# Kernel optimization log

Hardware: AMD Instinct MI355X
Metric: run time of the kernel (lower is better)

## Reference

```python
import jax, jax.numpy as jnp
import numpy as np

DIM = 96
EXPANSION = 2
INNER = DIM * EXPANSION        # 192
QKV_BLOCK = 4                  # per-head dim DH
NH = INNER // QKV_BLOCK        # 48 heads
CONV_K = 4
B, H, W = 2, 24, 24
EPS = 1e-5


def setup_inputs() -> dict:
    key = jax.random.key(0)
    ks = jax.random.split(key, 10)
    nrm = lambda k, shape, s=0.02: jax.random.normal(k, shape, dtype=jnp.float32) * s
    return {
        "x": jax.random.normal(ks[0], (B, DIM, H, W), dtype=jnp.float32),
        "ln_g": jnp.ones((DIM,), jnp.float32),
        "ln_b": jnp.zeros((DIM,), jnp.float32),
        "w_up": nrm(ks[1], (2 * INNER, DIM)),
        "b_up": jnp.zeros((2 * INNER,), jnp.float32),
        "w_q": nrm(ks[2], (NH, QKV_BLOCK, QKV_BLOCK), 0.2),
        "b_q": jnp.zeros((INNER,), jnp.float32),
        "w_k": nrm(ks[3], (NH, QKV_BLOCK, QKV_BLOCK), 0.2),
        "b_k": jnp.zeros((INNER,), jnp.float32),
        "w_v": nrm(ks[4], (NH, QKV_BLOCK, QKV_BLOCK), 0.2),
        "b_v": jnp.zeros((INNER,), jnp.float32),
        "w_conv": nrm(ks[5], (INNER, 1, CONV_K), 0.1),  # depthwise (O,I/g,K)
        "b_conv": jnp.zeros((INNER,), jnp.float32),
        "w_ig": nrm(ks[6], (NH, 3 * INNER)),
        "b_ig": jnp.zeros((NH,), jnp.float32),
        "w_fg": jnp.zeros((NH, 3 * INNER), jnp.float32),
        "b_fg": jnp.linspace(3.0, 6.0, NH, dtype=jnp.float32),  # xLSTM fgate bias init
        "on_g": jnp.ones((INNER,), jnp.float32),
        "on_b": jnp.zeros((INNER,), jnp.float32),
        "skip": jnp.ones((INNER,), jnp.float32),
        "w_down": nrm(ks[7], (DIM, INNER)),
        "b_down": jnp.zeros((DIM,), jnp.float32),
    }


def _layernorm(x, g, b):
    m = x.mean(-1, keepdims=True)
    v = x.var(-1, keepdims=True)
    return (x - m) / jnp.sqrt(v + EPS) * g + b


def _causal_conv(x, w, b):
    # x: (B,S,D); depthwise causal conv1d, left-pad K-1
    y = jax.lax.conv_general_dilated(
        x.transpose(0, 2, 1), w, (1,), [(CONV_K - 1, 0)],
        feature_group_count=INNER, dimension_numbers=("NCH", "OIH", "NCH"))
    return y.transpose(0, 2, 1) + b


def _headwise(x, w, b):
    # LinearHeadwiseExpand: block-diagonal per-head linear
    Bq, S, _ = x.shape
    xh = x.reshape(Bq, S, NH, QKV_BLOCK)
    return jnp.einsum("bsnd,nod->bsno", xh, w).reshape(Bq, S, INNER) + b


def _mlstm(q, k, v, ig, fg):
    # parallel_stabilized_simple; q,k,v: (B,NH,S,DH); ig,fg: (B,NH,S)
    S, DH = q.shape[2], q.shape[3]
    log_f = jax.nn.log_sigmoid(fg)                                           # (B,NH,S)
    lf_cum = jnp.concatenate(
        [jnp.zeros_like(log_f[..., :1]), jnp.cumsum(log_f, axis=-1)], axis=-1)  # (B,NH,S+1)
    log_fmat = lf_cum[..., :, None] - lf_cum[..., None, :]                   # (B,NH,S+1,S+1)
    ltr = jnp.tril(jnp.ones((S, S), dtype=bool))
    log_fg_mat = jnp.where(ltr, log_fmat[..., 1:, 1:], -jnp.inf)             # (B,NH,S,S)
    log_D = log_fg_mat + ig[..., None, :]
    max_log_D = jnp.max(log_D, axis=-1, keepdims=True)                       # rowwise stabilizer
    Dm = jnp.exp(log_D - max_log_D)
    qk = jnp.einsum("bhsd,bhtd->bhst", q, k) * (DH ** -0.5)
    Cm = qk * Dm
    normalizer = jnp.maximum(jnp.abs(Cm.sum(-1, keepdims=True)), jnp.exp(-max_log_D))
    return jnp.einsum("bhst,bhtd->bhsd", Cm / (normalizer + 1e-6), v)


def _mh_norm(h, g, b):
    # MultiHeadLayerNorm: per-head normalization over DH, then full affine
    m = h.mean(-1, keepdims=True)
    v = h.var(-1, keepdims=True)
    hn = (h - m) / jnp.sqrt(v + EPS)
    return hn * g.reshape(1, NH, 1, QKV_BLOCK) + b.reshape(1, NH, 1, QKV_BLOCK)


def reference(x, ln_g, ln_b, w_up, b_up, w_q, b_q, w_k, b_k, w_v, b_v,
              w_conv, b_conv, w_ig, b_ig, w_fg, b_fg, on_g, on_b, skip,
              w_down, b_down):
    Bb, C, Hh, Ww = x.shape
    S = Hh * Ww
    xs = x.reshape(Bb, C, S).transpose(0, 2, 1)                 # (B,S,C)
    h = _layernorm(xs, ln_g, ln_b)                              # ViLBlock pre-LN
    xi = h @ w_up.T + b_up                                      # (B,S,2*INNER)
    x_mlstm, z = jnp.split(xi, 2, axis=-1)
    x_conv = jax.nn.silu(_causal_conv(x_mlstm, w_conv, b_conv))
    q = _headwise(x_conv, w_q, b_q)
    k = _headwise(x_conv, w_k, b_k)
    v = _headwise(x_mlstm, w_v, b_v)
    qkv = jnp.concatenate([q, k, v], axis=-1)                   # (B,S,3*INNER)
    ig = jnp.einsum("bsf,hf->bhs", qkv, w_ig) + b_ig[None, :, None]
    fg = jnp.einsum("bsf,hf->bhs", qkv, w_fg) + b_fg[None, :, None]
    to_heads = lambda t: t.reshape(Bb, S, NH, QKV_BLOCK).transpose(0, 2, 1, 3)
    h_tilde = _mlstm(to_heads(q), to_heads(k), to_heads(v), ig, fg)   # (B,NH,S,DH)
    h_norm = _mh_norm(h_tilde, on_g, on_b).transpose(0, 2, 1, 3).reshape(Bb, S, INNER)
    h_skip = h_norm + skip * x_conv
    h_state = h_skip * jax.nn.silu(z)
    out = h_state @ w_down.T + b_down
    y = xs + out                                                # ViLBlock residual
    return y.transpose(0, 2, 1).reshape(Bb, C, Hh, Ww)
```

## Files before the change

kernel.cpp:

```cpp
#include <hip/hip_runtime.h>
#include <math.h>

#define SEQ   576
#define CDIM  96
#define INNER 192
#define NHEAD 48
#define DH    4
#define NB    2
#define EPSV  1e-5f
#define RT    64

__device__ __forceinline__ float silu_f(float x) { return x / (1.f + __expf(-x)); }
__device__ __forceinline__ float logsig_f(float x) {
    return (x >= 0.f) ? -log1pf(__expf(-x)) : (x - log1pf(__expf(x)));
}

__global__ void __launch_bounds__(512) k_ln_up(const float* __restrict__ x,
    const float* __restrict__ ln_g, const float* __restrict__ ln_b,
    const float* __restrict__ w_up, const float* __restrict__ b_up,
    float* __restrict__ xm, float* __restrict__ z) {
    const int t = threadIdx.x;
    const int p0 = blockIdx.x * 8;
    const int b = p0 / SEQ;
    const int f0 = blockIdx.y * 192;
    __shared__ __align__(16) float hbuf[8][CDIM];

    {
        const int p = t >> 6, l = t & 63;
        const int s = (p0 + p) % SEQ;
        const float v0 = x[(size_t)(b * CDIM + l) * SEQ + s];
        const float v1 = (l < 32) ? x[(size_t)(b * CDIM + 64 + l) * SEQ + s] : 0.f;
        float sum = v0 + v1, sq = v0 * v0 + v1 * v1;
        #pragma unroll
        for (int off = 1; off < 64; off <<= 1) {
            sum += __shfl_xor(sum, off);
            sq  += __shfl_xor(sq, off);
        }
        const float mean = sum * (1.f / CDIM);
        const float var = sq * (1.f / CDIM) - mean * mean;
        const float rstd = rsqrtf(var + EPSV);
        hbuf[p][l] = (v0 - mean) * rstd * ln_g[l] + ln_b[l];
        if (l < 32) hbuf[p][64 + l] = (v1 - mean) * rstd * ln_g[64 + l] + ln_b[64 + l];
    }
    __syncthreads();

    const int lane = t & 7, oi = t >> 3;
    const int p2 = oi & 7, fg = oi >> 3;
    const int pos = p0 + p2;
    const float4* hr = (const float4*)(&hbuf[p2][0]) + lane * 3;
    const float4 h0 = hr[0], h1 = hr[1], h2 = hr[2];
    #pragma unroll 4
    for (int j = 0; j < 24; ++j) {
        const int f = f0 + fg + 8 * j;
        const float4* wr = (const float4*)(w_up + (size_t)f * CDIM) + lane * 3;
        float4 w0 = wr[0], w1 = wr[1], w2 = wr[2];
        float acc = h0.x * w0.x + h0.y * w0.y + h0.z * w0.z + h0.w * w0.w
                  + h1.x * w1.x + h1.y * w1.y + h1.z * w1.z + h1.w * w1.w
                  + h2.x * w2.x + h2.y * w2.y + h2.z * w2.z + h2.w * w2.w;
        #pragma unroll
        for (int off = 1; off < 8; off <<= 1) acc += __shfl_xor(acc, off);
        if (lane == 0) {
            acc += b_up[f];
            if (f < INNER) xm[(size_t)pos * INNER + f] = acc;
            else           z [(size_t)pos * INNER + (f - INNER)] = acc;
        }
    }
}

__global__ void __launch_bounds__(512) k_conv_qkv_gates(const float* __restrict__ xm,
    const float* __restrict__ w_conv, const float* __restrict__ b_conv,
    const float* __restrict__ w_q, const float* __restrict__ b_q,
    const float* __restrict__ w_k, const float* __restrict__ b_k,
    const float* __restrict__ w_v, const float* __restrict__ b_v,
    const float* __restrict__ w_ig, const float* __restrict__ b_ig,
    const float* __restrict__ w_fg, const float* __restrict__ b_fg,
    float* __restrict__ xc, float* __restrict__ qw, float* __restrict__ kw,
    float* __restrict__ vw, float* __restrict__ igw, float* __restrict__ fgw) {
    const int t = threadIdx.x;
    const int p0 = blockIdx.x * 4;
    const int b = p0 / SEQ, s0 = p0 % SEQ;
    __shared__ float xmb[7][INNER];
    __shared__ float xcb[4][INNER];
    __shared__ __align__(16) float qkvb[4][3 * INNER];

    for (int i = t; i < 7 * INNER; i += 512) {
        const int r = i / INNER, c = i % INNER;
        const int ss = s0 - 3 + r;
        xmb[r][c] = (ss >= 0) ? xm[(size_t)(b * SEQ + ss) * INNER + c] : 0.f;
    }
    __syncthreads();

    for (int i = t; i < 4 * INNER; i += 512) {
        const int p = i / INNER, c = i % INNER;
        float acc = b_conv[c];
        #pragma unroll
        for (int j = 0; j < 4; ++j) acc += xmb[p + j][c] * w_conv[c * 4 + j];
        const float v = silu_f(acc);
        xcb[p][c] = v;
        xc[(size_t)(b * SEQ + s0 + p) * INNER + c] = v;
    }
    __syncthreads();

    for (int i = t; i < 4 * INNER; i += 512) {
        const int p = i / INNER, c = i % INNER;
        const int n = c >> 2, o = c & 3;
        const float* wq = w_q + n * 16 + o * 4;
        const float* wk = w_k + n * 16 + o * 4;
        const float* wv = w_v + n * 16 + o * 4;
        float q = b_q[c], k = b_k[c], v = b_v[c];
        #pragma unroll
        for (int dd = 0; dd < 4; ++dd) {
            q += xcb[p][n * 4 + dd] * wq[dd];
            k += xcb[p][n * 4 + dd] * wk[dd];
            v += xmb[p + 3][n * 4 + dd] * wv[dd];
        }
        qkvb[p][c] = q; qkvb[p][INNER + c] = k; qkvb[p][2 * INNER + c] = v;
        const size_t base = ((size_t)(b * NHEAD + n) * SEQ + s0 + p) * DH + o;
        qw[base] = q; kw[base] = k; vw[base] = v;
    }
    __syncthreads();

    {
        const int w = t >> 6;
        const int l16 = t & 15, gg = (t >> 4) & 3;
        #pragma unroll
        for (int it = 0; it < 3; ++it) {
            const int g = w * 12 + it * 4 + gg;
            const bool isfg = (g >= NHEAD);
            const int hh = isfg ? (g - NHEAD) : g;
            const float4* wr = (const float4*)((isfg ? w_fg : w_ig) + (size_t)hh * (3 * INNER)) + l16 * 9;
            float4 wf[9];
            #pragma unroll
            for (int j = 0; j < 9; ++j) wf[j] = wr[j];
            #pragma unroll
            for (int p = 0; p < 4; ++p) {
                const float4* xr = (const float4*)(&qkvb[p][0]) + l16 * 9;
                float acc = 0.f;
                #pragma unroll
                for (int j = 0; j < 9; ++j) {
                    const float4 a = xr[j];
                    acc += a.x * wf[j].x + a.y * wf[j].y + a.z * wf[j].z + a.w * wf[j].w;
                }
                #pragma unroll
                for (int off = 1; off < 16; off <<= 1) acc += __shfl_xor(acc, off);
                if (l16 == 0) {
                    acc += isfg ? b_fg[hh] : b_ig[hh];
                    (isfg ? fgw : igw)[((size_t)b * NHEAD + hh) * SEQ + s0 + p] = acc;
                }
            }
        }
    }
}

__global__ void __launch_bounds__(256) k_mlstm(const float* __restrict__ qw,
    const float* __restrict__ kw, const float* __restrict__ vw,
    const float* __restrict__ igw, const float* __restrict__ fgw,
    float* __restrict__ ht) {
    const int bh = blockIdx.x;
    const int r0 = blockIdx.y * RT;
    const int nt = r0 + RT;
    const int t = threadIdx.x;
    __shared__ float4 k4[SEQ], v4[SEQ];
    __shared__ float m_l[SEQ], M_l[SEQ], lfc_l[SEQ];

    const float4* kb = (const float4*)(kw + (size_t)bh * SEQ * DH);
    const float4* vb = (const float4*)(vw + (size_t)bh * SEQ * DH);
    for (int i = t; i < nt; i += 256) { k4[i] = kb[i]; v4[i] = vb[i]; }

    if (t < 64) {
        const int base = t * 9;
        float pre[9], mv[9], mx[9];
        float run = 0.f;
        #pragma unroll
        for (int j = 0; j < 9; ++j) {
            run += logsig_f(fgw[(size_t)bh * SEQ + base + j]);
            pre[j] = run;
        }
        float incl = run;
        #pragma unroll
        for (int off = 1; off < 64; off <<= 1) {
            float o = __shfl_up(incl, off);
            if (t >= off) incl += o;
        }
        const float excl = incl - run;
        float runm = -INFINITY;
        #pragma unroll
        for (int j = 0; j < 9; ++j) {
            float lfc = excl + pre[j];
            lfc_l[base + j] = lfc;
            float mt = igw[(size_t)bh * SEQ + base + j] - lfc;
            mv[j] = mt;
            runm = fmaxf(runm, mt);
            mx[j] = runm;
        }
        float sc = runm;
        #pragma unroll
        for (int off = 1; off < 64; off <<= 1) {
            float o = __shfl_up(sc, off);
            if (t >= off) sc = fmaxf(sc, o);
        }
        float exclm = __shfl_up(sc, 1);
        if (t == 0) exclm = -INFINITY;
        #pragma unroll
        for (int j = 0; j < 9; ++j) {
            m_l[base + j] = mv[j];
            M_l[base + j] = fmaxf(exclm, mx[j]);
        }
    }
    __syncthreads();

    const int sub = t & 3;
    const int s0 = r0 + (t >> 2);
    const float4 q = ((const float4*)(qw + (size_t)bh * SEQ * DH))[s0];
    const float Ms = M_l[s0], lfcs = lfc_l[s0];

    float a0 = 0.f, a1 = 0.f, a2 = 0.f, a3 = 0.f, csum = 0.f;
    for (int tt = sub; tt <= s0; tt += 4) {
        float e = __expf(m_l[tt] - Ms);
        float4 kk = k4[tt], vv = v4[tt];
        float qk = q.x * kk.x + q.y * kk.y + q.z * kk.z + q.w * kk.w;
        float c = qk * 0.5f * e;
        csum += c;
        a0 += c * vv.x; a1 += c * vv.y; a2 += c * vv.z; a3 += c * vv.w;
    }
    #pragma unroll
    for (int off = 1; off < 4; off <<= 1) {
        csum += __shfl_xor(csum, off);
        a0 += __shfl_xor(a0, off); a1 += __shfl_xor(a1, off);
        a2 += __shfl_xor(a2, off); a3 += __shfl_xor(a3, off);
    }
    const float floorv = __expf(-(lfcs + Ms));
    const float inv = 1.f / (fmaxf(fabsf(csum), floorv) + 1e-6f);
    const float val = (sub == 0) ? a0 : (sub == 1) ? a1 : (sub == 2) ? a2 : a3;
    ht[((size_t)bh * SEQ + s0) * 4 + sub] = val * inv;
}

__global__ void __launch_bounds__(512) k_epi(const float* __restrict__ ht,
    const float* __restrict__ on_g, const float* __restrict__ on_b,
    const float* __restrict__ skip, const float* __restrict__ xc,
    const float* __restrict__ zz, const float* __restrict__ w_down,
    const float* __restrict__ b_down, const float* __restrict__ x,
    float* __restrict__ out) {
    const int t = threadIdx.x;
    const int p0 = blockIdx.x * 4;
    const int b = p0 / SEQ;
    __shared__ __align__(16) float hs[4][INNER];

    for (int i = t; i < 4 * INNER; i += 512) {
        const int p = i / INNER, c = i % INNER;
        const int pos = p0 + p, s = pos % SEQ;
        const int n = c >> 2, o = c & 3;
        const float4 hv = ((const float4*)ht)[(size_t)(b * NHEAD + n) * SEQ + s];
        const float mean = (hv.x + hv.y + hv.z + hv.w) * 0.25f;
        const float d0 = hv.x - mean, d1 = hv.y - mean, d2 = hv.z - mean, d3 = hv.w - mean;
        const float var = (d0 * d0 + d1 * d1 + d2 * d2 + d3 * d3) * 0.25f;
        const float rstd = rsqrtf(var + EPSV);
        const float he = (o == 0) ? hv.x : (o == 1) ? hv.y : (o == 2) ? hv.z : hv.w;
        const float hn = (he - mean) * rstd * on_g[c] + on_b[c];
        const float hk = hn + skip[c] * xc[(size_t)pos * INNER + c];
        hs[p][c] = hk * silu_f(zz[(size_t)pos * INNER + c]);
    }
    __syncthreads();

    const int lane = t & 7, oi = t >> 3;
    const int p2 = oi & 3, cg = oi >> 2;
    const int pos = p0 + p2, s = pos % SEQ;
    const float4* hr = (const float4*)(&hs[p2][0]) + lane * 6;
    float4 h4[6];
    #pragma unroll
    for (int j = 0; j < 6; ++j) h4[j] = hr[j];
    #pragma unroll
    for (int j = 0; j < 6; ++j) {
        const int c = cg + 16 * j;
        const float4* wr = (const float4*)(w_down + (size_t)c * INNER) + lane * 6;
        float acc = 0.f;
        #pragma unroll
        for (int u = 0; u < 6; ++u) {
            const float4 w = wr[u];
            acc += h4[u].x * w.x + h4[u].y * w.y + h4[u].z * w.z + h4[u].w * w.w;
        }
        #pragma unroll
        for (int off = 1; off < 8; off <<= 1) acc += __shfl_xor(acc, off);
        if (lane == 0) {
            const size_t idx = ((size_t)b * CDIM + c) * SEQ + s;
            out[idx] = x[idx] + acc + b_down[c];
        }
    }
}

extern "C" void kernel_launch(void* const* d_in, const int* in_sizes, int n_in,
                              void* d_out, int out_size, void* d_ws, size_t ws_size,
                              hipStream_t stream) {
    const float* x      = (const float*)d_in[0];
    const float* ln_g   = (const float*)d_in[1];
    const float* ln_b   = (const float*)d_in[2];
    const float* w_up   = (const float*)d_in[3];
    const float* b_up   = (const float*)d_in[4];
    const float* w_q    = (const float*)d_in[5];
    const float* b_q    = (const float*)d_in[6];
    const float* w_k    = (const float*)d_in[7];
    const float* b_k    = (const float*)d_in[8];
    const float* w_v    = (const float*)d_in[9];
    const float* b_v    = (const float*)d_in[10];
    const float* w_conv = (const float*)d_in[11];
    const float* b_conv = (const float*)d_in[12];
    const float* w_ig   = (const float*)d_in[13];
    const float* b_ig   = (const float*)d_in[14];
    const float* w_fg   = (const float*)d_in[15];
    const float* b_fg   = (const float*)d_in[16];
    const float* on_g   = (const float*)d_in[17];
    const float* on_b   = (const float*)d_in[18];
    const float* skip   = (const float*)d_in[19];
    const float* w_down = (const float*)d_in[20];
    const float* b_down = (const float*)d_in[21];

    float* ws = (float*)d_ws;
    const size_t NSI = (size_t)NB * SEQ * INNER;
    const size_t NHS = (size_t)NB * NHEAD * SEQ;
    float* xm  = ws;
    float* z   = xm + NSI;
    float* xc  = z + NSI;
    float* qw  = xc + NSI;
    float* kw  = qw + NSI;
    float* vw  = kw + NSI;
    float* igw = vw + NSI;
    float* fgw = igw + NHS;
    float* ht  = fgw + NHS;

    float* out = (float*)d_out;

    hipLaunchKernelGGL(k_ln_up, dim3(NB * SEQ / 8, 2), dim3(512), 0, stream,
                       x, ln_g, ln_b, w_up, b_up, xm, z);
    hipLaunchKernelGGL(k_conv_qkv_gates, dim3(NB * SEQ / 4), dim3(512), 0, stream,
                       xm, w_conv, b_conv, w_q, b_q, w_k, b_k, w_v, b_v,
                       w_ig, b_ig, w_fg, b_fg, xc, qw, kw, vw, igw, fgw);
    hipLaunchKernelGGL(k_mlstm, dim3(NB * NHEAD, SEQ / RT), dim3(256), 0, stream,
                       qw, kw, vw, igw, fgw, ht);
    hipLaunchKernelGGL(k_epi, dim3(NB * SEQ / 4), dim3(512), 0, stream,
                       ht, on_g, on_b, skip, xc, z, w_down, b_down, x, out);
}
```

Baseline: 60.31 us.

## Fuse four stages into one persistent cooperative kernel with grid syncs

Merges the LN+up-projection, conv/qkv/gates, mLSTM and epilogue kernels into a single cooperative kernel of 288 blocks separated by grid.sync(), removing three launch gaps. The mLSTM phase is rebalanced so each block handles three row tiles of one head, chosen so every block gets a roughly equal share of the causal triangle. Each stage now runs on fewer, smaller blocks (256 threads), and grid-wide barriers add their own cost, so per-stage parallelism drops.

```diff
diff --git a/kernel.cpp b/kernel.cpp
--- a/kernel.cpp
+++ b/kernel.cpp
@@ -1,4 +1,5 @@
 #include <hip/hip_runtime.h>
+#include <hip/hip_cooperative_groups.h>
 #include <math.h>
 
 #define SEQ   576
@@ -8,282 +9,280 @@
 #define DH    4
 #define NB    2
 #define EPSV  1e-5f
-#define RT    64
+
+namespace cg = cooperative_groups;
 
 __device__ __forceinline__ float silu_f(float x) { return x / (1.f + __expf(-x)); }
 __device__ __forceinline__ float logsig_f(float x) {
     return (x >= 0.f) ? -log1pf(__expf(-x)) : (x - log1pf(__expf(x)));
 }
 
-__global__ void __launch_bounds__(512) k_ln_up(const float* __restrict__ x,
-    const float* __restrict__ ln_g, const float* __restrict__ ln_b,
-    const float* __restrict__ w_up, const float* __restrict__ b_up,
-    float* __restrict__ xm, float* __restrict__ z) {
+struct Params {
+    const float *x, *ln_g, *ln_b, *w_up, *b_up;
+    const float *w_q, *b_q, *w_k, *b_k, *w_v, *b_v;
+    const float *w_conv, *b_conv;
+    const float *w_ig, *b_ig, *w_fg, *b_fg;
+    const float *on_g, *on_b, *skip, *w_down, *b_down;
+    float *xm, *z, *xc, *qw, *kw, *vw, *igw, *fgw, *ht, *out;
+};
+
+__global__ void __launch_bounds__(256, 2) k_vil(Params P) {
     const int t = threadIdx.x;
-    const int p0 = blockIdx.x * 8;
-    const int b = p0 / SEQ;
-    const int f0 = blockIdx.y * 192;
-    __shared__ __align__(16) float hbuf[8][CDIM];
+    const int blk = blockIdx.x;
+    __shared__ __align__(16) float smem[6336];
+    cg::grid_group grid = cg::this_grid();
 
     {
-        const int p = t >> 6, l = t & 63;
-        const int s = (p0 + p) % SEQ;
-        const float v0 = x[(size_t)(b * CDIM + l) * SEQ + s];
-        const float v1 = (l < 32) ? x[(size_t)(b * CDIM + 64 + l) * SEQ + s] : 0.f;
-        float sum = v0 + v1, sq = v0 * v0 + v1 * v1;
+        float* hbuf = smem;
+        const int p0 = blk * 4;
+        const int b = p0 / SEQ;
+        {
+            const int p = t >> 6, l = t & 63;
+            const int s = (p0 + p) % SEQ;
+            const float v0 = P.x[(size_t)(b * CDIM + l) * SEQ + s];
+            const float v1 = (l < 32) ? P.x[(size_t)(b * CDIM + 64 + l) * SEQ + s] : 0.f;
+            float sum = v0 + v1, sq = v0 * v0 + v1 * v1;
+            #pragma unroll
+            for (int off = 1; off < 64; off <<= 1) {
+                sum += __shfl_xor(sum, off);
+                sq  += __shfl_xor(sq, off);
+            }
+            const float mean = sum * (1.f / CDIM);
+            const float rstd = rsqrtf(sq * (1.f / CDIM) - mean * mean + EPSV);
+            hbuf[p * CDIM + l] = (v0 - mean) * rstd * P.ln_g[l] + P.ln_b[l];
+            if (l < 32) hbuf[p * CDIM + 64 + l] = (v1 - mean) * rstd * P.ln_g[64 + l] + P.ln_b[64 + l];
+        }
+        __syncthreads();
+        const int lane = t & 7, oi = t >> 3;
+        const int p2 = oi & 3, fg = oi >> 2;
+        const int pos = p0 + p2;
+        const float4* hr = (const float4*)(hbuf + p2 * CDIM) + lane * 3;
+        const float4 h0 = hr[0], h1 = hr[1], h2 = hr[2];
+        #pragma unroll 4
+        for (int j = 0; j < 48; ++j) {
+            const int f = fg + 8 * j;
+            const float4* wr = (const float4*)(P.w_up + (size_t)f * CDIM) + lane * 3;
+            const float4 w0 = wr[0], w1 = wr[1], w2 = wr[2];
+            float acc = h0.x*w0.x + h0.y*w0.y + h0.z*w0.z + h0.w*w0.w
+                      + h1.x*w1.x + h1.y*w1.y + h1.z*w1.z + h1.w*w1.w
+                      + h2.x*w2.x + h2.y*w2.y + h2.z*w2.z + h2.w*w2.w;
+            #pragma unroll
+            for (int off = 1; off < 8; off <<= 1) acc += __shfl_xor(acc, off);
+            if (lane == 0) {
+                acc += P.b_up[f];
+                if (f < INNER) P.xm[(size_t)pos * INNER + f] = acc;
+                else           P.z [(size_t)pos * INNER + (f - INNER)] = acc;
+            }
+        }
+    }
+    grid.sync();
+
+    {
+        float* xmb  = smem;
+        float* xcb  = smem + 7 * INNER;
+        float* qkvb = smem + 11 * INNER;
+        const int p0 = blk * 4;
+        const int b = p0 / SEQ, s0 = p0 % SEQ;
+
+        for (int i = t; i < 7 * INNER; i += 256) {
+            const int r = i / INNER, c = i % INNER;
+            const int ss = s0 - 3 + r;
+            xmb[i] = (ss >= 0) ? P.xm[(size_t)(b * SEQ + ss) * INNER + c] : 0.f;
+        }
+        __syncthreads();
+        for (int i = t; i < 4 * INNER; i += 256) {
+            const int p = i / INNER, c = i % INNER;
+            float acc = P.b_conv[c];
+            #pragma unroll
+            for (int j = 0; j < 4; ++j) acc += xmb[(p + j) * INNER + c] * P.w_conv[c * 4 + j];
+            const float v = silu_f(acc);
+            xcb[i] = v;
+            P.xc[(size_t)(p0 + p) * INNER + c] = v;
+        }
+        __syncthreads();
+        for (int i = t; i < 4 * INNER; i += 256) {
+            const int p = i / INNER, c = i % INNER;
+            const int n = c >> 2, o = c & 3;
+            const float* wq = P.w_q + n * 16 + o * 4;
+            const float* wk = P.w_k + n * 16 + o * 4;
+            const float* wv = P.w_v + n * 16 + o * 4;
+            float q = P.b_q[c], k = P.b_k[c], v = P.b_v[c];
+            #pragma unroll
+            for (int dd = 0; dd < 4; ++dd) {
+                q += xcb[p * INNER + n * 4 + dd] * wq[dd];
+                k += xcb[p * INNER + n * 4 + dd] * wk[dd];
+                v += xmb[(p + 3) * INNER + n * 4 + dd] * wv[dd];
+            }
+            qkvb[p * 576 + c] = q; qkvb[p * 576 + INNER + c] = k; qkvb[p * 576 + 2 * INNER + c] = v;
+            const size_t base = ((size_t)(b * NHEAD + n) * SEQ + s0 + p) * DH + o;
+            P.qw[base] = q; P.kw[base] = k; P.vw[base] = v;
+        }
+        __syncthreads();
+        {
+            const int w = t >> 6, l16 = t & 15, gg = (t >> 4) & 3;
+            #pragma unroll
+            for (int it = 0; it < 6; ++it) {
+                const int g = w * 24 + it * 4 + gg;
+                const bool isfg = (g >= NHEAD);
+                const int hh = isfg ? (g - NHEAD) : g;
+                const float4* wr = (const float4*)((isfg ? P.w_fg : P.w_ig) + (size_t)hh * 576) + l16 * 9;
+                float4 wf[9];
+                #pragma unroll
+                for (int j = 0; j < 9; ++j) wf[j] = wr[j];
+                #pragma unroll
+                for (int p = 0; p < 4; ++p) {
+                    const float4* xr = (const float4*)(qkvb + p * 576) + l16 * 9;
+                    float acc = 0.f;
+                    #pragma unroll
+                    for (int j = 0; j < 9; ++j) {
+                        const float4 a = xr[j];
+                        acc += a.x * wf[j].x + a.y * wf[j].y + a.z * wf[j].z + a.w * wf[j].w;
+                    }
+                    #pragma unroll
+                    for (int off = 1; off < 16; off <<= 1) acc += __shfl_xor(acc, off);
+                    if (l16 == 0) {
+                        acc += isfg ? P.b_fg[hh] : P.b_ig[hh];
+                        (isfg ? P.fgw : P.igw)[((size_t)b * NHEAD + hh) * SEQ + s0 + p] = acc;
+                    }
+                }
+            }
+        }
+    }
+    grid.sync();
+
+    {
+        float4* k4 = (float4*)smem;
+        float4* v4 = (float4*)(smem + 2304);
+        float* m_l = smem + 4608;
+        float* M_l = smem + 5184;
+        float* lfc_l = smem + 5760;
+        const int bh = blk % 96, g = blk / 96;
+        const int ntmax = (g == 0) ? 576 : (g == 1 ? 448 : 512);
+
+        const float4* kb = (const float4*)(P.kw + (size_t)bh * SEQ * DH);
+        const float4* vb = (const float4*)(P.vw + (size_t)bh * SEQ * DH);
+        for (int i = t; i < ntmax; i += 256) { k4[i] = kb[i]; v4[i] = vb[i]; }
+
+        if (t < 64) {
+            const int base = t * 9;
+            float pre[9], mv[9], mx[9];
+            float run = 0.f;
+            #pragma unroll
+            for (int j = 0; j < 9; ++j) {
+                run += logsig_f(P.fgw[(size_t)bh * SEQ + base + j]);
+                pre[j] = run;
+            }
+            float incl = run;
+            #pragma unroll
+            for (int off = 1; off < 64; off <<= 1) {
+                float o = __shfl_up(incl, off);
+                if (t >= off) incl += o;
+            }
+            const float excl = incl - run;
+            float runm = -INFINITY;
+            #pragma unroll
+            for (int j = 0; j < 9; ++j) {
+                float lfc = excl + pre[j];
+                lfc_l[base + j] = lfc;
+                float mt = P.igw[(size_t)bh * SEQ + base + j] - lfc;
+                mv[j] = mt;
+                runm = fmaxf(runm, mt);
+                mx[j] = runm;
+            }
+            float sc = runm;
+            #pragma unroll
+            for (int off = 1; off < 64; off <<= 1) {
+                float o = __shfl_up(sc, off);
+                if (t >= off) sc = fmaxf(sc, o);
+            }
+            float exclm = __shfl_up(sc, 1);
+            if (t == 0) exclm = -INFINITY;
+            #pragma unroll
+            for (int j = 0; j < 9; ++j) {
+                m_l[base + j] = mv[j];
+                M_l[base + j] = fmaxf(exclm, mx[j]);
+            }
+        }
+        __syncthreads();
+
+        const int lane = t & 7, rr = t >> 3;
         #pragma unroll
-        for (int off = 1; off < 64; off <<= 1) {
-            sum += __shfl_xor(sum, off);
-            sq  += __shfl_xor(sq, off);
-        }
-        const float mean = sum * (1.f / CDIM);
-        const float var = sq * (1.f / CDIM) - mean * mean;
-        const float rstd = rsqrtf(var + EPSV);
-        hbuf[p][l] = (v0 - mean) * rstd * ln_g[l] + ln_b[l];
-        if (l < 32) hbuf[p][64 + l] = (v1 - mean) * rstd * ln_g[64 + l] + ln_b[64 + l];
-    }
-    __syncthreads();
-
-    const int lane = t & 7, oi = t >> 3;
-    const int p2 = oi & 7, fg = oi >> 3;
-    const int pos = p0 + p2;
-    const float4* hr = (const float4*)(&hbuf[p2][0]) + lane * 3;
-    const float4 h0 = hr[0], h1 = hr[1], h2 = hr[2];
-    #pragma unroll 4
-    for (int j = 0; j < 24; ++j) {
-        const int f = f0 + fg + 8 * j;
-        const float4* wr = (const float4*)(w_up + (size_t)f * CDIM) + lane * 3;
-        float4 w0 = wr[0], w1 = wr[1], w2 = wr[2];
-        float acc = h0.x * w0.x + h0.y * w0.y + h0.z * w0.z + h0.w * w0.w
-                  + h1.x * w1.x + h1.y * w1.y + h1.z * w1.z + h1.w * w1.w
-                  + h2.x * w2.x + h2.y * w2.y + h2.z * w2.z + h2.w * w2.w;
-        #pragma unroll
-        for (int off = 1; off < 8; off <<= 1) acc += __shfl_xor(acc, off);
-        if (lane == 0) {
-            acc += b_up[f];
-            if (f < INNER) xm[(size_t)pos * INNER + f] = acc;
-            else           z [(size_t)pos * INNER + (f - INNER)] = acc;
-        }
-    }
-}
-
-__global__ void __launch_bounds__(512) k_conv_qkv_gates(const float* __restrict__ xm,
-    const float* __restrict__ w_conv, const float* __restrict__ b_conv,
-    const float* __restrict__ w_q, const float* __restrict__ b_q,
-    const float* __restrict__ w_k, const float* __restrict__ b_k,
-    const float* __restrict__ w_v, const float* __restrict__ b_v,
-    const float* __restrict__ w_ig, const float* __restrict__ b_ig,
-    const float* __restrict__ w_fg, const float* __restrict__ b_fg,
-    float* __restrict__ xc, float* __restrict__ qw, float* __restrict__ kw,
-    float* __restrict__ vw, float* __restrict__ igw, float* __restrict__ fgw) {
-    const int t = threadIdx.x;
-    const int p0 = blockIdx.x * 4;
-    const int b = p0 / SEQ, s0 = p0 % SEQ;
-    __shared__ float xmb[7][INNER];
-    __shared__ float xcb[4][INNER];
-    __shared__ __align__(16) float qkvb[4][3 * INNER];
-
-    for (int i = t; i < 7 * INNER; i += 512) {
-        const int r = i / INNER, c = i % INNER;
-        const int ss = s0 - 3 + r;
-        xmb[r][c] = (ss >= 0) ? xm[(size_t)(b * SEQ + ss) * INNER + c] : 0.f;
-    }
-    __syncthreads();
-
-    for (int i = t; i < 4 * INNER; i += 512) {
-        const int p = i / INNER, c = i % INNER;
-        float acc = b_conv[c];
-        #pragma unroll
-        for (int j = 0; j < 4; ++j) acc += xmb[p + j][c] * w_conv[c * 4 + j];
-        const float v = silu_f(acc);
-        xcb[p][c] = v;
-        xc[(size_t)(b * SEQ + s0 + p) * INNER + c] = v;
-    }
-    __syncthreads();
-
-    for (int i = t; i < 4 * INNER; i += 512) {
-        const int p = i / INNER, c = i % INNER;
-        const int n = c >> 2, o = c & 3;
-        const float* wq = w_q + n * 16 + o * 4;
-        const float* wk = w_k + n * 16 + o * 4;
-        const float* wv = w_v + n * 16 + o * 4;
-        float q = b_q[c], k = b_k[c], v = b_v[c];
-        #pragma unroll
-        for (int dd = 0; dd < 4; ++dd) {
-            q += xcb[p][n * 4 + dd] * wq[dd];
-            k += xcb[p][n * 4 + dd] * wk[dd];
-            v += xmb[p + 3][n * 4 + dd] * wv[dd];
-        }
-        qkvb[p][c] = q; qkvb[p][INNER + c] = k; qkvb[p][2 * INNER + c] = v;
-        const size_t base = ((size_t)(b * NHEAD + n) * SEQ + s0 + p) * DH + o;
-        qw[base] = q; kw[base] = k; vw[base] = v;
-    }
-    __syncthreads();
-
-    {
-        const int w = t >> 6;
-        const int l16 = t & 15, gg = (t >> 4) & 3;
-        #pragma unroll
-        for (int it = 0; it < 3; ++it) {
-            const int g = w * 12 + it * 4 + gg;
-            const bool isfg = (g >= NHEAD);
-            const int hh = isfg ? (g - NHEAD) : g;
-            const float4* wr = (const float4*)((isfg ? w_fg : w_ig) + (size_t)hh * (3 * INNER)) + l16 * 9;
-            float4 wf[9];
-            #pragma unroll
-            for (int j = 0; j < 9; ++j) wf[j] = wr[j];
-            #pragma unroll
-            for (int p = 0; p < 4; ++p) {
-                const float4* xr = (const float4*)(&qkvb[p][0]) + l16 * 9;
-                float acc = 0.f;
-                #pragma unroll
-                for (int j = 0; j < 9; ++j) {
-                    const float4 a = xr[j];
-                    acc += a.x * wf[j].x + a.y * wf[j].y + a.z * wf[j].z + a.w * wf[j].w;
+        for (int ti = 0; ti < 3; ++ti) {
+            const int tile = (ti == 0) ? ((g == 0) ? 0 : (g == 1) ? 1 : 2)
+                           : (ti == 1) ? ((g == 0) ? 4 : (g == 1) ? 5 : 3)
+                                       : ((g == 0) ? 8 : (g == 1) ? 6 : 7);
+            #pragma unroll
+            for (int half = 0; half < 2; ++half) {
+                const int row = tile * 64 + rr + half * 32;
+                const float4 q = ((const float4*)(P.qw + (size_t)bh * SEQ * DH))[row];
+                const float Ms = M_l[row], lfcs = lfc_l[row];
+                float a0 = 0.f, a1 = 0.f, a2 = 0.f, a3 = 0.f, csum = 0.f;
+                for (int tt = lane; tt <= row; tt += 8) {
+                    const float e = __expf(m_l[tt] - Ms);
+                    const float4 kk = k4[tt], vv = v4[tt];
+                    const float c = (q.x*kk.x + q.y*kk.y + q.z*kk.z + q.w*kk.w) * 0.5f * e;
+                    csum += c;
+                    a0 += c * vv.x; a1 += c * vv.y; a2 += c * vv.z; a3 += c * vv.w;
                 }
                 #pragma unroll
-                for (int off = 1; off < 16; off <<= 1) acc += __shfl_xor(acc, off);
-                if (l16 == 0) {
-                    acc += isfg ? b_fg[hh] : b_ig[hh];
-                    (isfg ? fgw : igw)[((size_t)b * NHEAD + hh) * SEQ + s0 + p] = acc;
+                for (int off = 1; off < 8; off <<= 1) {
+                    csum += __shfl_xor(csum, off);
+                    a0 += __shfl_xor(a0, off); a1 += __shfl_xor(a1, off);
+                    a2 += __shfl_xor(a2, off); a3 += __shfl_xor(a3, off);
                 }
+                if (lane == 0) {
+                    const float floorv = __expf(-(lfcs + Ms));
+                    const float inv = 1.f / (fmaxf(fabsf(csum), floorv) + 1e-6f);
+                    ((float4*)P.ht)[(size_t)bh * SEQ + row] =
+                        make_float4(a0 * inv, a1 * inv, a2 * inv, a3 * inv);
+                }
             }
         }
     }
-}
-
-__global__ void __launch_bounds__(256) k_mlstm(const float* __restrict__ qw,
-    const float* __restrict__ kw, const float* __restrict__ vw,
-    const float* __restrict__ igw, const float* __restrict__ fgw,
-    float* __restrict__ ht) {
-    const int bh = blockIdx.x;
-    const int r0 = blockIdx.y * RT;
-    const int nt = r0 + RT;
-    const int t = threadIdx.x;
-    __shared__ float4 k4[SEQ], v4[SEQ];
-    __shared__ float m_l[SEQ], M_l[SEQ], lfc_l[SEQ];
-
-    const float4* kb = (const float4*)(kw + (size_t)bh * SEQ * DH);
-    const float4* vb = (const float4*)(vw + (size_t)bh * SEQ * DH);
-    for (int i = t; i < nt; i += 256) { k4[i] = kb[i]; v4[i] = vb[i]; }
-
-    if (t < 64) {
-        const int base = t * 9;
-        float pre[9], mv[9], mx[9];
-        float run = 0.f;
+    grid.sync();
+
+    {
+        float* hs = smem;
+        const int p0 = blk * 4;
+        const int b = p0 / SEQ;
+        for (int i = t; i < 4 * INNER; i += 256) {
+            const int p = i / INNER, c = i % INNER;
+            const int pos = p0 + p, s = pos % SEQ;
+            const int n = c >> 2, o = c & 3;
+            const float4 hv = ((const float4*)P.ht)[(size_t)(b * NHEAD + n) * SEQ + s];
+            const float mean = (hv.x + hv.y + hv.z + hv.w) * 0.25f;
+            const float d0 = hv.x - mean, d1 = hv.y - mean, d2 = hv.z - mean, d3 = hv.w - mean;
+            const float var = (d0*d0 + d1*d1 + d2*d2 + d3*d3) * 0.25f;
+            const float rstd = rsqrtf(var + EPSV);
+            const float he = (o == 0) ? hv.x : (o == 1) ? hv.y : (o == 2) ? hv.z : hv.w;
+            const float hn = (he - mean) * rstd * P.on_g[c] + P.on_b[c];
+            const float hk = hn + P.skip[c] * P.xc[(size_t)pos * INNER + c];
+            hs[i] = hk * silu_f(P.z[(size_t)pos * INNER + c]);
+        }
+        __syncthreads();
+        const int lane = t & 7, oi = t >> 3;
+        const int p2 = oi & 3, cg2 = oi >> 2;
+        const int pos = p0 + p2, s = pos % SEQ;
+        const float4* hr = (const float4*)(hs + p2 * INNER) + lane * 6;
+        float4 h4[6];
         #pragma unroll
-        for (int j = 0; j < 9; ++j) {
-            run += logsig_f(fgw[(size_t)bh * SEQ + base + j]);
-            pre[j] = run;
-        }
-        float incl = run;
+        for (int j = 0; j < 6; ++j) h4[j] = hr[j];
         #pragma unroll
-        for (int off = 1; off < 64; off <<= 1) {
-            float o = __shfl_up(incl, off);
-            if (t >= off) incl += o;
-        }
-        const float excl = incl - run;
-        float runm = -INFINITY;
-        #pragma unroll
-        for (int j = 0; j < 9; ++j) {
-            float lfc = excl + pre[j];
-            lfc_l[base + j] = lfc;
-            float mt = igw[(size_t)bh * SEQ + base + j] - lfc;
-            mv[j] = mt;
-            runm = fmaxf(runm, mt);
-            mx[j] = runm;
-        }
-        float sc = runm;
-        #pragma unroll
-        for (int off = 1; off < 64; off <<= 1) {
-            float o = __shfl_up(sc, off);
-            if (t >= off) sc = fmaxf(sc, o);
-        }
-        float exclm = __shfl_up(sc, 1);
-        if (t == 0) exclm = -INFINITY;
-        #pragma unroll
-        for (int j = 0; j < 9; ++j) {
-            m_l[base + j] = mv[j];
-            M_l[base + j] = fmaxf(exclm, mx[j]);
-        }
-    }
-    __syncthreads();
-
-    const int sub = t & 3;
-    const int s0 = r0 + (t >> 2);
-    const float4 q = ((const float4*)(qw + (size_t)bh * SEQ * DH))[s0];
-    const float Ms = M_l[s0], lfcs = lfc_l[s0];
-
-    float a0 = 0.f, a1 = 0.f, a2 = 0.f, a3 = 0.f, csum = 0.f;
-    for (int tt = sub; tt <= s0; tt += 4) {
-        float e = __expf(m_l[tt] - Ms);
-        float4 kk = k4[tt], vv = v4[tt];
-        float qk = q.x * kk.x + q.y * kk.y + q.z * kk.z + q.w * kk.w;
-        float c = qk * 0.5f * e;
-        csum += c;
-        a0 += c * vv.x; a1 += c * vv.y; a2 += c * vv.z; a3 += c * vv.w;
-    }
-    #pragma unroll
-    for (int off = 1; off < 4; off <<= 1) {
-        csum += __shfl_xor(csum, off);
-        a0 += __shfl_xor(a0, off); a1 += __shfl_xor(a1, off);
-        a2 += __shfl_xor(a2, off); a3 += __shfl_xor(a3, off);
-    }
-    const float floorv = __expf(-(lfcs + Ms));
-    const float inv = 1.f / (fmaxf(fabsf(csum), floorv) + 1e-6f);
-    const float val = (sub == 0) ? a0 : (sub == 1) ? a1 : (sub == 2) ? a2 : a3;
-    ht[((size_t)bh * SEQ + s0) * 4 + sub] = val * inv;
-}
-
-__global__ void __launch_bounds__(512) k_epi(const float* __restrict__ ht,
-    const float* __restrict__ on_g, const float* __restrict__ on_b,
-    const float* __restrict__ skip, const float* __restrict__ xc,
-    const float* __restrict__ zz, const float* __restrict__ w_down,
-    const float* __restrict__ b_down, const float* __restrict__ x,
-    float* __restrict__ out) {
-    const int t = threadIdx.x;
-    const int p0 = blockIdx.x * 4;
-    const int b = p0 / SEQ;
-    __shared__ __align__(16) float hs[4][INNER];
-
-    for (int i = t; i < 4 * INNER; i += 512) {
-        const int p = i / INNER, c = i % INNER;
-        const int pos = p0 + p, s = pos % SEQ;
-        const int n = c >> 2, o = c & 3;
-        const float4 hv = ((const float4*)ht)[(size_t)(b * NHEAD + n) * SEQ + s];
-        const float mean = (hv.x + hv.y + hv.z + hv.w) * 0.25f;
-        const float d0 = hv.x - mean, d1 = hv.y - mean, d2 = hv.z - mean, d3 = hv.w - mean;
-        const float var = (d0 * d0 + d1 * d1 + d2 * d2 + d3 * d3) * 0.25f;
-        const float rstd = rsqrtf(var + EPSV);
-        const float he = (o == 0) ? hv.x : (o == 1) ? hv.y : (o == 2) ? hv.z : hv.w;
-        const float hn = (he - mean) * rstd * on_g[c] + on_b[c];
-        const float hk = hn + skip[c] * xc[(size_t)pos * INNER + c];
-        hs[p][c] = hk * silu_f(zz[(size_t)pos * INNER + c]);
-    }
-    __syncthreads();
-
-    const int lane = t & 7, oi = t >> 3;
-    const int p2 = oi & 3, cg = oi >> 2;
-    const int pos = p0 + p2, s = pos % SEQ;
-    const float4* hr = (const float4*)(&hs[p2][0]) + lane * 6;
-    float4 h4[6];
-    #pragma unroll
-    for (int j = 0; j < 6; ++j) h4[j] = hr[j];
-    #pragma unroll
-    for (int j = 0; j < 6; ++j) {
-        const int c = cg + 16 * j;
-        const float4* wr = (const float4*)(w_down + (size_t)c * INNER) + lane * 6;
-        float acc = 0.f;
-        #pragma unroll
-        for (int u = 0; u < 6; ++u) {
-            const float4 w = wr[u];
-            acc += h4[u].x * w.x + h4[u].y * w.y + h4[u].z * w.z + h4[u].w * w.w;
-        }
-        #pragma unroll
-        for (int off = 1; off < 8; off <<= 1) acc += __shfl_xor(acc, off);
-        if (lane == 0) {
-            const size_t idx = ((size_t)b * CDIM + c) * SEQ + s;
-            out[idx] = x[idx] + acc + b_down[c];
+        for (int j = 0; j < 12; ++j) {
+            const int c = cg2 + 8 * j;
+            const float4* wr = (const float4*)(P.w_down + (size_t)c * INNER) + lane * 6;
+            float acc = 0.f;
+            #pragma unroll
+            for (int u = 0; u < 6; ++u) {
+                const float4 w = wr[u];
+                acc += h4[u].x*w.x + h4[u].y*w.y + h4[u].z*w.z + h4[u].w*w.w;
+            }
+            #pragma unroll
+            for (int off = 1; off < 8; off <<= 1) acc += __shfl_xor(acc, off);
+            if (lane == 0) {
+                const size_t idx = ((size_t)b * CDIM + c) * SEQ + s;
+                P.out[idx] = P.x[idx] + acc + P.b_down[c];
+            }
         }
     }
 }
@@ -291,51 +290,45 @@
 extern "C" void kernel_launch(void* const* d_in, const int* in_sizes, int n_in,
                               void* d_out, int out_size, void* d_ws, size_t ws_size,
                               hipStream_t stream) {
-    const float* x      = (const float*)d_in[0];
-    const float* ln_g   = (const float*)d_in[1];
-    const float* ln_b   = (const float*)d_in[2];
-    const float* w_up   = (const float*)d_in[3];
-    const float* b_up   = (const float*)d_in[4];
-    const float* w_q    = (const float*)d_in[5];
-    const float* b_q    = (const float*)d_in[6];
-    const float* w_k    = (const float*)d_in[7];
-    const float* b_k    = (const float*)d_in[8];
-    const float* w_v    = (const float*)d_in[9];
-    const float* b_v    = (const float*)d_in[10];
-    const float* w_conv = (const float*)d_in[11];
-    const float* b_conv = (const float*)d_in[12];
-    const float* w_ig   = (const float*)d_in[13];
-    const float* b_ig   = (const float*)d_in[14];
-    const float* w_fg   = (const float*)d_in[15];
-    const float* b_fg   = (const float*)d_in[16];
-    const float* on_g   = (const float*)d_in[17];
-    const float* on_b   = (const float*)d_in[18];
-    const float* skip   = (const float*)d_in[19];
-    const float* w_down = (const float*)d_in[20];
-    const float* b_down = (const float*)d_in[21];
-
     float* ws = (float*)d_ws;
     const size_t NSI = (size_t)NB * SEQ * INNER;
     const size_t NHS = (size_t)NB * NHEAD * SEQ;
-    float* xm  = ws;
-    float* z   = xm + NSI;
-    float* xc  = z + NSI;
-    float* qw  = xc + NSI;
-    float* kw  = qw + NSI;
-    float* vw  = kw + NSI;
-    float* igw = vw + NSI;
-    float* fgw = igw + NHS;
-    float* ht  = fgw + NHS;
-
-    float* out = (float*)d_out;
-
-    hipLaunchKernelGGL(k_ln_up, dim3(NB * SEQ / 8, 2), dim3(512), 0, stream,
-                       x, ln_g, ln_b, w_up, b_up, xm, z);
-    hipLaunchKernelGGL(k_conv_qkv_gates, dim3(NB * SEQ / 4), dim3(512), 0, stream,
-                       xm, w_conv, b_conv, w_q, b_q, w_k, b_k, w_v, b_v,
-                       w_ig, b_ig, w_fg, b_fg, xc, qw, kw, vw, igw, fgw);
-    hipLaunchKernelGGL(k_mlstm, dim3(NB * NHEAD, SEQ / RT), dim3(256), 0, stream,
-                       qw, kw, vw, igw, fgw, ht);
-    hipLaunchKernelGGL(k_epi, dim3(NB * SEQ / 4), dim3(512), 0, stream,
-                       ht, on_g, on_b, skip, xc, z, w_down, b_down, x, out);
+
+    Params P;
+    P.x      = (const float*)d_in[0];
+    P.ln_g   = (const float*)d_in[1];
+    P.ln_b   = (const float*)d_in[2];
+    P.w_up   = (const float*)d_in[3];
+    P.b_up   = (const float*)d_in[4];
+    P.w_q    = (const float*)d_in[5];
+    P.b_q    = (const float*)d_in[6];
+    P.w_k    = (const float*)d_in[7];
+    P.b_k    = (const float*)d_in[8];
+    P.w_v    = (const float*)d_in[9];
+    P.b_v    = (const float*)d_in[10];
+    P.w_conv = (const float*)d_in[11];
+    P.b_conv = (const float*)d_in[12];
+    P.w_ig   = (const float*)d_in[13];
+    P.b_ig   = (const float*)d_in[14];
+    P.w_fg   = (const float*)d_in[15];
+    P.b_fg   = (const float*)d_in[16];
+    P.on_g   = (const float*)d_in[17];
+    P.on_b   = (const float*)d_in[18];
+    P.skip   = (const float*)d_in[19];
+    P.w_down = (const float*)d_in[20];
+    P.b_down = (const float*)d_in[21];
+
+    P.xm  = ws;
+    P.z   = P.xm + NSI;
+    P.xc  = P.z + NSI;
+    P.qw  = P.xc + NSI;
+    P.kw  = P.qw + NSI;
+    P.vw  = P.kw + NSI;
+    P.igw = P.vw + NSI;
+    P.fgw = P.igw + NHS;
+    P.ht  = P.fgw + NHS;
+    P.out = (float*)d_out;
+
+    void* args[] = { (void*)&P };
+    hipLaunchCooperativeKernel((void*)k_vil, dim3(288), dim3(256), args, 0, stream);
 }
```

After: 188.9 us. +213.3%, slower.

## Fuse LayerNorm/up-projection into conv-QKV-gates kernel with halo recompute

Applied to the files above, without the earlier changes.

Merges the LN + up-projection kernel with the conv/QKV/gate kernel. Each block now handles 8 positions and recomputes the x_mlstm half for a 3-row causal halo (11 rows) in shared memory, so xm no longer goes through global memory and one launch is removed. The cost is redundant up-projection work on halo rows (about 11/8), fewer blocks (144 instead of 288/576), and more shared memory per block, which can lower occupancy.

```diff
diff --git a/kernel.cpp b/kernel.cpp
--- a/kernel.cpp
+++ b/kernel.cpp
@@ -15,93 +15,97 @@
     return (x >= 0.f) ? -log1pf(__expf(-x)) : (x - log1pf(__expf(x)));
 }
 
-__global__ void __launch_bounds__(512) k_ln_up(const float* __restrict__ x,
+__global__ void __launch_bounds__(512) k_front(const float* __restrict__ x,
     const float* __restrict__ ln_g, const float* __restrict__ ln_b,
     const float* __restrict__ w_up, const float* __restrict__ b_up,
-    float* __restrict__ xm, float* __restrict__ z) {
-    const int t = threadIdx.x;
-    const int p0 = blockIdx.x * 8;
-    const int b = p0 / SEQ;
-    const int f0 = blockIdx.y * 192;
-    __shared__ __align__(16) float hbuf[8][CDIM];
-
-    {
-        const int p = t >> 6, l = t & 63;
-        const int s = (p0 + p) % SEQ;
-        const float v0 = x[(size_t)(b * CDIM + l) * SEQ + s];
-        const float v1 = (l < 32) ? x[(size_t)(b * CDIM + 64 + l) * SEQ + s] : 0.f;
-        float sum = v0 + v1, sq = v0 * v0 + v1 * v1;
-        #pragma unroll
-        for (int off = 1; off < 64; off <<= 1) {
-            sum += __shfl_xor(sum, off);
-            sq  += __shfl_xor(sq, off);
-        }
-        const float mean = sum * (1.f / CDIM);
-        const float var = sq * (1.f / CDIM) - mean * mean;
-        const float rstd = rsqrtf(var + EPSV);
-        hbuf[p][l] = (v0 - mean) * rstd * ln_g[l] + ln_b[l];
-        if (l < 32) hbuf[p][64 + l] = (v1 - mean) * rstd * ln_g[64 + l] + ln_b[64 + l];
-    }
-    __syncthreads();
-
-    const int lane = t & 7, oi = t >> 3;
-    const int p2 = oi & 7, fg = oi >> 3;
-    const int pos = p0 + p2;
-    const float4* hr = (const float4*)(&hbuf[p2][0]) + lane * 3;
-    const float4 h0 = hr[0], h1 = hr[1], h2 = hr[2];
-    #pragma unroll 4
-    for (int j = 0; j < 24; ++j) {
-        const int f = f0 + fg + 8 * j;
-        const float4* wr = (const float4*)(w_up + (size_t)f * CDIM) + lane * 3;
-        float4 w0 = wr[0], w1 = wr[1], w2 = wr[2];
-        float acc = h0.x * w0.x + h0.y * w0.y + h0.z * w0.z + h0.w * w0.w
-                  + h1.x * w1.x + h1.y * w1.y + h1.z * w1.z + h1.w * w1.w
-                  + h2.x * w2.x + h2.y * w2.y + h2.z * w2.z + h2.w * w2.w;
-        #pragma unroll
-        for (int off = 1; off < 8; off <<= 1) acc += __shfl_xor(acc, off);
-        if (lane == 0) {
-            acc += b_up[f];
-            if (f < INNER) xm[(size_t)pos * INNER + f] = acc;
-            else           z [(size_t)pos * INNER + (f - INNER)] = acc;
-        }
-    }
-}
-
-__global__ void __launch_bounds__(512) k_conv_qkv_gates(const float* __restrict__ xm,
     const float* __restrict__ w_conv, const float* __restrict__ b_conv,
     const float* __restrict__ w_q, const float* __restrict__ b_q,
     const float* __restrict__ w_k, const float* __restrict__ b_k,
     const float* __restrict__ w_v, const float* __restrict__ b_v,
     const float* __restrict__ w_ig, const float* __restrict__ b_ig,
     const float* __restrict__ w_fg, const float* __restrict__ b_fg,
-    float* __restrict__ xc, float* __restrict__ qw, float* __restrict__ kw,
-    float* __restrict__ vw, float* __restrict__ igw, float* __restrict__ fgw) {
+    float* __restrict__ z, float* __restrict__ xc,
+    float* __restrict__ qw, float* __restrict__ kw, float* __restrict__ vw,
+    float* __restrict__ igw, float* __restrict__ fgw) {
     const int t = threadIdx.x;
-    const int p0 = blockIdx.x * 4;
+    const int p0 = blockIdx.x * 8;
     const int b = p0 / SEQ, s0 = p0 % SEQ;
-    __shared__ float xmb[7][INNER];
-    __shared__ float xcb[4][INNER];
-    __shared__ __align__(16) float qkvb[4][3 * INNER];
-
-    for (int i = t; i < 7 * INNER; i += 512) {
-        const int r = i / INNER, c = i % INNER;
-        const int ss = s0 - 3 + r;
-        xmb[r][c] = (ss >= 0) ? xm[(size_t)(b * SEQ + ss) * INNER + c] : 0.f;
-    }
-    __syncthreads();
-
-    for (int i = t; i < 4 * INNER; i += 512) {
+    __shared__ __align__(16) float hbuf[11 * CDIM];
+    __shared__ __align__(16) float xmb[11 * INNER];
+    __shared__ __align__(16) float xcb[8 * INNER];
+    __shared__ __align__(16) float qkvb[8 * 576];
+
+    {
+        const int wv = t >> 6, l = t & 63;
+        for (int ph = wv; ph < 11; ph += 8) {
+            const int ss = s0 - 3 + ph;
+            if (ss < 0) continue;
+            const float v0 = x[(size_t)(b * CDIM + l) * SEQ + ss];
+            const float v1 = (l < 32) ? x[(size_t)(b * CDIM + 64 + l) * SEQ + ss] : 0.f;
+            float sum = v0 + v1, sq = v0 * v0 + v1 * v1;
+            #pragma unroll
+            for (int off = 1; off < 64; off <<= 1) {
+                sum += __shfl_xor(sum, off);
+                sq  += __shfl_xor(sq, off);
+            }
+            const float mean = sum * (1.f / CDIM);
+            const float rstd = rsqrtf(sq * (1.f / CDIM) - mean * mean + EPSV);
+            hbuf[ph * CDIM + l] = (v0 - mean) * rstd * ln_g[l] + ln_b[l];
+            if (l < 32) hbuf[ph * CDIM + 64 + l] = (v1 - mean) * rstd * ln_g[64 + l] + ln_b[64 + l];
+        }
+    }
+    __syncthreads();
+
+    const int lane = t & 7, oi = t >> 3;
+    #pragma unroll 3
+    for (int j = 0; j < 33; ++j) {
+        const int idx = j * 64 + oi;
+        const int ph = idx / INNER, f = idx % INNER;
+        const int ss = s0 - 3 + ph;
+        if (ss < 0) {
+            if (lane == 0) xmb[ph * INNER + f] = 0.f;
+            continue;
+        }
+        const float4* hr = (const float4*)(hbuf + ph * CDIM) + lane * 3;
+        const float4* wr = (const float4*)(w_up + (size_t)f * CDIM) + lane * 3;
+        const float4 h0 = hr[0], h1 = hr[1], h2 = hr[2];
+        const float4 w0 = wr[0], w1 = wr[1], w2 = wr[2];
+        float acc = h0.x*w0.x + h0.y*w0.y + h0.z*w0.z + h0.w*w0.w
+                  + h1.x*w1.x + h1.y*w1.y + h1.z*w1.z + h1.w*w1.w
+                  + h2.x*w2.x + h2.y*w2.y + h2.z*w2.z + h2.w*w2.w;
+        #pragma unroll
+        for (int off = 1; off < 8; off <<= 1) acc += __shfl_xor(acc, off);
+        if (lane == 0) xmb[ph * INNER + f] = acc + b_up[f];
+    }
+    #pragma unroll 3
+    for (int j = 0; j < 24; ++j) {
+        const int idx = j * 64 + oi;
+        const int ph = 3 + idx / INNER, f = idx % INNER;
+        const float4* hr = (const float4*)(hbuf + ph * CDIM) + lane * 3;
+        const float4* wr = (const float4*)(w_up + (size_t)(INNER + f) * CDIM) + lane * 3;
+        const float4 h0 = hr[0], h1 = hr[1], h2 = hr[2];
+        const float4 w0 = wr[0], w1 = wr[1], w2 = wr[2];
+        float acc = h0.x*w0.x + h0.y*w0.y + h0.z*w0.z + h0.w*w0.w
+                  + h1.x*w1.x + h1.y*w1.y + h1.z*w1.z + h1.w*w1.w
+                  + h2.x*w2.x + h2.y*w2.y + h2.z*w2.z + h2.w*w2.w;
+        #pragma unroll
+        for (int off = 1; off < 8; off <<= 1) acc += __shfl_xor(acc, off);
+        if (lane == 0) z[(size_t)(p0 + ph - 3) * INNER + f] = acc + b_up[INNER + f];
+    }
+    __syncthreads();
+
+    for (int i = t; i < 8 * INNER; i += 512) {
         const int p = i / INNER, c = i % INNER;
         float acc = b_conv[c];
         #pragma unroll
-        for (int j = 0; j < 4; ++j) acc += xmb[p + j][c] * w_conv[c * 4 + j];
+        for (int j = 0; j < 4; ++j) acc += xmb[(p + j) * INNER + c] * w_conv[c * 4 + j];
         const float v = silu_f(acc);
-        xcb[p][c] = v;
-        xc[(size_t)(b * SEQ + s0 + p) * INNER + c] = v;
-    }
-    __syncthreads();
-
-    for (int i = t; i < 4 * INNER; i += 512) {
+        xcb[i] = v;
+        xc[(size_t)(p0 + p) * INNER + c] = v;
+    }
+    __syncthreads();
+
+    for (int i = t; i < 8 * INNER; i += 512) {
         const int p = i / INNER, c = i % INNER;
         const int n = c >> 2, o = c & 3;
         const float* wq = w_q + n * 16 + o * 4;
@@ -110,31 +114,30 @@
         float q = b_q[c], k = b_k[c], v = b_v[c];
         #pragma unroll
         for (int dd = 0; dd < 4; ++dd) {
-            q += xcb[p][n * 4 + dd] * wq[dd];
-            k += xcb[p][n * 4 + dd] * wk[dd];
-            v += xmb[p + 3][n * 4 + dd] * wv[dd];
-        }
-        qkvb[p][c] = q; qkvb[p][INNER + c] = k; qkvb[p][2 * INNER + c] = v;
+            q += xcb[p * INNER + n * 4 + dd] * wq[dd];
+            k += xcb[p * INNER + n * 4 + dd] * wk[dd];
+            v += xmb[(p + 3) * INNER + n * 4 + dd] * wv[dd];
+        }
+        qkvb[p * 576 + c] = q; qkvb[p * 576 + INNER + c] = k; qkvb[p * 576 + 2 * INNER + c] = v;
         const size_t base = ((size_t)(b * NHEAD + n) * SEQ + s0 + p) * DH + o;
         qw[base] = q; kw[base] = k; vw[base] = v;
     }
     __syncthreads();
 
     {
-        const int w = t >> 6;
-        const int l16 = t & 15, gg = (t >> 4) & 3;
+        const int w = t >> 6, l16 = t & 15, gg = (t >> 4) & 3;
         #pragma unroll
         for (int it = 0; it < 3; ++it) {
             const int g = w * 12 + it * 4 + gg;
             const bool isfg = (g >= NHEAD);
             const int hh = isfg ? (g - NHEAD) : g;
-            const float4* wr = (const float4*)((isfg ? w_fg : w_ig) + (size_t)hh * (3 * INNER)) + l16 * 9;
+            const float4* wr = (const float4*)((isfg ? w_fg : w_ig) + (size_t)hh * 576) + l16 * 9;
             float4 wf[9];
             #pragma unroll
             for (int j = 0; j < 9; ++j) wf[j] = wr[j];
             #pragma unroll
-            for (int p = 0; p < 4; ++p) {
-                const float4* xr = (const float4*)(&qkvb[p][0]) + l16 * 9;
+            for (int p = 0; p < 8; ++p) {
+                const float4* xr = (const float4*)(qkvb + p * 576) + l16 * 9;
                 float acc = 0.f;
                 #pragma unroll
                 for (int j = 0; j < 9; ++j) {
@@ -253,7 +256,7 @@
         const float4 hv = ((const float4*)ht)[(size_t)(b * NHEAD + n) * SEQ + s];
         const float mean = (hv.x + hv.y + hv.z + hv.w) * 0.25f;
         const float d0 = hv.x - mean, d1 = hv.y - mean, d2 = hv.z - mean, d3 = hv.w - mean;
-        const float var = (d0 * d0 + d1 * d1 + d2 * d2 + d3 * d3) * 0.25f;
+        const float var = (d0*d0 + d1*d1 + d2*d2 + d3*d3) * 0.25f;
         const float rstd = rsqrtf(var + EPSV);
         const float he = (o == 0) ? hv.x : (o == 1) ? hv.y : (o == 2) ? hv.z : hv.w;
         const float hn = (he - mean) * rstd * on_g[c] + on_b[c];
@@ -263,7 +266,7 @@
     __syncthreads();
 
     const int lane = t & 7, oi = t >> 3;
-    const int p2 = oi & 3, cg = oi >> 2;
+    const int p2 = oi & 3, cg2 = oi >> 2;
     const int pos = p0 + p2, s = pos % SEQ;
     const float4* hr = (const float4*)(&hs[p2][0]) + lane * 6;
     float4 h4[6];
@@ -271,13 +274,13 @@
     for (int j = 0; j < 6; ++j) h4[j] = hr[j];
     #pragma unroll
     for (int j = 0; j < 6; ++j) {
-        const int c = cg + 16 * j;
+        const int c = cg2 + 16 * j;
         const float4* wr = (const float4*)(w_down + (size_t)c * INNER) + lane * 6;
         float acc = 0.f;
         #pragma unroll
         for (int u = 0; u < 6; ++u) {
             const float4 w = wr[u];
-            acc += h4[u].x * w.x + h4[u].y * w.y + h4[u].z * w.z + h4[u].w * w.w;
+            acc += h4[u].x*w.x + h4[u].y*w.y + h4[u].z*w.z + h4[u].w*w.w;
         }
         #pragma unroll
         for (int off = 1; off < 8; off <<= 1) acc += __shfl_xor(acc, off);
@@ -317,8 +320,7 @@
     float* ws = (float*)d_ws;
     const size_t NSI = (size_t)NB * SEQ * INNER;
     const size_t NHS = (size_t)NB * NHEAD * SEQ;
-    float* xm  = ws;
-    float* z   = xm + NSI;
+    float* z   = ws;
     float* xc  = z + NSI;
     float* qw  = xc + NSI;
     float* kw  = qw + NSI;
@@ -329,11 +331,10 @@
 
     float* out = (float*)d_out;
 
-    hipLaunchKernelGGL(k_ln_up, dim3(NB * SEQ / 8, 2), dim3(512), 0, stream,
-                       x, ln_g, ln_b, w_up, b_up, xm, z);
-    hipLaunchKernelGGL(k_conv_qkv_gates, dim3(NB * SEQ / 4), dim3(512), 0, stream,
-                       xm, w_conv, b_conv, w_q, b_q, w_k, b_k, w_v, b_v,
-                       w_ig, b_ig, w_fg, b_fg, xc, qw, kw, vw, igw, fgw);
+    hipLaunchKernelGGL(k_front, dim3(NB * SEQ / 8), dim3(512), 0, stream,
+                       x, ln_g, ln_b, w_up, b_up, w_conv, b_conv,
+                       w_q, b_q, w_k, b_k, w_v, b_v, w_ig, b_ig, w_fg, b_fg,
+                       z, xc, qw, kw, vw, igw, fgw);
     hipLaunchKernelGGL(k_mlstm, dim3(NB * NHEAD, SEQ / RT), dim3(256), 0, stream,
                        qw, kw, vw, igw, fgw, ht);
     hipLaunchKernelGGL(k_epi, dim3(NB * SEQ / 4), dim3(512), 0, stream,
```

New measurement: 72.51 us. 20.2% more time.
